# Kernel optimization log

Hardware: AMD Instinct MI355X
Metric: run time of the kernel (lower is better)

## Reference

```python
import jax, jax.numpy as jnp
import numpy as np

N = 40000   # query points
M = 40000   # support points
H = 32      # neighbors per query
CIN = 64
COUT = 64
KS = 3      # kernel points per dim
PDIM = 3
K = KS ** PDIM  # 27 kernel points
RADIUS = 1.0
KP_EXTENT = RADIUS / (KS - 1) * PDIM ** 0.5


def _kernel_points():
    # replicates KPConv.getKernelPoints: grid of KS^PDIM points in a ball of RADIUS
    xyz = np.linspace(-1.0, 1.0, KS)
    pts = np.meshgrid(*PDIM * [xyz])
    pts = np.vstack([p.flatten() for p in pts]).T  # [K, PDIM]
    pts = pts / PDIM ** 0.5
    return (pts * RADIUS).astype(np.float32)


def setup_inputs() -> dict:
    key = jax.random.key(0)
    k1, k2, k3, k4, k5 = jax.random.split(key, 5)
    q_pts = jax.random.uniform(k1, (N, PDIM), dtype=jnp.float32) * 10.0
    s_pts = jax.random.uniform(k2, (M, PDIM), dtype=jnp.float32) * 10.0
    neighb_inds = jax.random.randint(k3, (N, H), 0, M + 1)  # M == shadow index
    x = jax.random.normal(k4, (M, CIN), dtype=jnp.float32)
    # kaiming-uniform-like init for weights [K, CIN, COUT]
    bound = (6.0 / ((1.0 + 5.0) * CIN)) ** 0.5
    weights = jax.random.uniform(k5, (K, CIN, COUT), dtype=jnp.float32,
                                 minval=-bound, maxval=bound)
    kernel_points = jnp.asarray(_kernel_points())
    return {"q_pts": q_pts, "s_pts": s_pts, "neighb_inds": neighb_inds,
            "x": x, "weights": weights, "kernel_points": kernel_points}


def reference(q_pts, s_pts, neighb_inds, x, weights, kernel_points):
    # append shadow support point (far away) and zero shadow feature
    s_pts_p = jnp.concatenate(
        [s_pts, jnp.full((1, s_pts.shape[-1]), 1e6, dtype=s_pts.dtype)], axis=0)
    x_p = jnp.concatenate(
        [x, jnp.zeros((1, x.shape[-1]), dtype=x.dtype)], axis=0)

    neighbors = s_pts_p[neighb_inds] - q_pts[:, None, :]        # [N, H, 3]
    neighb_x = x_p[neighb_inds]                                  # [N, H, CIN]

    # distance of each neighbor to each kernel point
    diff = neighbors[:, :, None, :] - kernel_points              # [N, H, K, 3]
    sq_d = jnp.sum(diff * diff, axis=-1)                         # [N, H, K]
    all_w = jnp.clip(1.0 - jnp.sqrt(sq_d) / KP_EXTENT, 0.0)      # [N, H, K]

    # all_weights^T @ neighb_x  -> [N, K, CIN]
    weighted = jnp.einsum('nhk,nhc->nkc', all_w, neighb_x)
    # per-kernel-point matmul with weights [K, CIN, COUT], summed over K
    out = jnp.einsum('nkc,kco->no', weighted, weights)           # [N, COUT]
    return out
```

## Files before the change

### kernel.cpp

```cpp
#include <hip/hip_runtime.h>

typedef short bf16x8 __attribute__((ext_vector_type(8)));
typedef float f32x4  __attribute__((ext_vector_type(4)));

#define HN    32
#define CIN   64
#define KP    27
#define QB    64
#define CAPB  96
#define NTB   1024
#define OSTR  65

#define QB2   32
#define CAP2  64
#define OSTR2 68

#define INV_EXT 1.1547005383792517f
#define CUT2    3.4821f

__device__ __forceinline__ unsigned f2bf(float f){
    union{float fv;unsigned u;}v; v.fv=f;
    unsigned u=v.u;
    u += 0x7fffu + ((u>>16)&1u);
    return u>>16;
}

__global__ __launch_bounds__(256)
void kp_prep2(const float* __restrict__ s, const float* __restrict__ W,
              float4* __restrict__ o, unsigned short* __restrict__ Wt2, int M)
{
    int tid = blockIdx.x*256 + threadIdx.x;
    if (tid < M) o[tid] = make_float4(s[tid*3+0], s[tid*3+1], s[tid*3+2], 0.f);
    if (tid < KP*8*64){
        int lane = tid & 63;
        int f  = (tid>>6) & 7;
        int kk = tid >> 9;
        int ot = f>>1, ks = f&1, gg = lane>>4;
        unsigned r[8];
#pragma unroll
        for (int j=0;j<8;++j)
            r[j] = f2bf(W[(size_t)kk*4096 + (size_t)(ks*32 + gg*8 + j)*64 + ot*16 + (lane&15)]);
        uint4 v; v.x=r[0]|(r[1]<<16); v.y=r[2]|(r[3]<<16); v.z=r[4]|(r[5]<<16); v.w=r[6]|(r[7]<<16);
        *(uint4*)&Wt2[(size_t)tid*8] = v;
    }
}

__device__ __forceinline__ void loadB(const unsigned short* __restrict__ Wt2, int k, int lane,
                                      bf16x8 (&b)[8]){
    const unsigned short* base = Wt2 + ((size_t)(k*8)*64 + lane)*8;
#pragma unroll
    for (int f=0;f<8;++f) b[f] = *(const bf16x8*)(base + f*512);
}
__device__ __forceinline__ void loadB_w(const float* __restrict__ W, int k, int lane, int g,
                                        bf16x8 (&b)[8]){
#pragma unroll
    for (int f=0;f<8;++f){
        int ot=f>>1, ks=f&1;
        union{unsigned u[4]; bf16x8 v;} bb;
#pragma unroll
        for (int jj=0;jj<4;++jj){
            unsigned l0=f2bf(W[(size_t)k*4096 + (size_t)(ks*32+g*8+2*jj)*64   + ot*16+(lane&15)]);
            unsigned l1=f2bf(W[(size_t)k*4096 + (size_t)(ks*32+g*8+2*jj+1)*64 + ot*16+(lane&15)]);
            bb.u[jj]=l0|(l1<<16);
        }
        b[f]=bb.v;
    }
}

__global__ __launch_bounds__(256,4)
void kpconv_fused(const float* __restrict__ q_pts, const int* __restrict__ inds,
                  const float* __restrict__ x, const float* __restrict__ kpts,
                  const float4* __restrict__ sp4, const unsigned short* __restrict__ Wt2,
                  float* __restrict__ out, int N, int M)
{
    __shared__ unsigned short rows[64*CIN];
    __shared__ __align__(16) float wlds[KP*64];
    __shared__ __align__(16) float outacc[QB2*OSTR2];
    __shared__ float qls[QB2*3];
    __shared__ float bx[CAP2], by[CAP2], bz[CAP2];
    __shared__ int bq[CAP2], bixs[CAP2];
    __shared__ int cnt;

    const int t    = threadIdx.x;
    const int lane = t & 63;
    const int wv   = t >> 6;
    const int g    = lane >> 4;
    const int r15  = lane & 15;
    const int nq0  = blockIdx.x * QB2;
    const int NP   = N*HN;

    for (int j=t; j<QB2*OSTR2; j+=256) outacc[j]=0.f;
    for (int j=t; j<QB2*3;    j+=256){ int gi=nq0*3+j; qls[j]=(gi<N*3)? q_pts[gi]:0.f; }
    if (t < CAP2) bq[t]=0;
    if (t==0) cnt=0;
    __syncthreads();

    int idxv[4];
#pragma unroll
    for (int jj=0; jj<4; ++jj){
        int pair = nq0*HN + jj*256 + t;
        idxv[jj] = (pair < NP) ? inds[pair] : M;
    }
    float4 s4v[4];
#pragma unroll
    for (int jj=0; jj<4; ++jj){
        int ic = (idxv[jj] < M) ? idxv[jj] : 0;
        s4v[jj] = sp4[ic];
    }
#pragma unroll
    for (int jj=0; jj<4; ++jj){
        if (idxv[jj] < M){
            int q = (jj*256 + t) >> 5;
            float px=s4v[jj].x-qls[q*3], py=s4v[jj].y-qls[q*3+1], pz=s4v[jj].z-qls[q*3+2];
            if (px*px+py*py+pz*pz <= CUT2){
                int sl = atomicAdd(&cnt, 1);
                if (sl < CAP2){ bx[sl]=px; by[sl]=py; bz[sl]=pz; bq[sl]=q; bixs[sl]=idxv[jj]; }
            }
        }
    }
    __syncthreads();
    const int total = cnt;

    auto process = [&](int cc){
        const int nrow = (cc + 15) & ~15;
        int itA=t, itB=t+256;
        int rlA=itA>>3, c8A=itA&7, rlB=itB>>3, c8B=itB&7;
        bool vA=(rlA<cc), vB=(rlB<cc);
        bool wrA=(rlA<nrow), wrB=(rlB<nrow);
        int ixA = vA ? bixs[rlA] : bixs[0];
        int ixB = vB ? bixs[rlB] : bixs[0];
        const float4* xrA = (const float4*)(x + (size_t)ixA*CIN);
        const float4* xrB = (const float4*)(x + (size_t)ixB*CIN);
        float4 fA0=xrA[c8A*2], fA1=xrA[c8A*2+1];
        float4 fB0=xrB[c8B*2], fB1=xrB[c8B*2+1];
        for (int i=t; i<KP*64; i+=256){
            int row = i&63;
            if (row >= nrow) continue;
            int k = i>>6;
            float w=0.f;
            if (row < cc){
                float dx=bx[row]-kpts[k*3+0];
                float dy=by[row]-kpts[k*3+1];
                float dz=bz[row]-kpts[k*3+2];
                w = fmaxf(1.f - sqrtf(dx*dx+dy*dy+dz*dz)*INV_EXT, 0.f);
            }
            wlds[i]=w;
        }
        if (wrA){
            uint4 v; v.x=0u; v.y=0u; v.z=0u; v.w=0u;
            if (vA){
                v.x=f2bf(fA0.x)|(f2bf(fA0.y)<<16); v.y=f2bf(fA0.z)|(f2bf(fA0.w)<<16);
                v.z=f2bf(fA1.x)|(f2bf(fA1.y)<<16); v.w=f2bf(fA1.z)|(f2bf(fA1.w)<<16);
            }
            *(uint4*)((char*)rows + rlA*128 + ((c8A*16)^((rlA&7)<<4))) = v;
        }
        if (wrB){
            uint4 v; v.x=0u; v.y=0u; v.z=0u; v.w=0u;
            if (vB){
                v.x=f2bf(fB0.x)|(f2bf(fB0.y)<<16); v.y=f2bf(fB0.z)|(f2bf(fB0.w)<<16);
                v.z=f2bf(fB1.x)|(f2bf(fB1.y)<<16); v.w=f2bf(fB1.z)|(f2bf(fB1.w)<<16);
            }
            *(uint4*)((char*)rows + rlB*128 + ((c8B*16)^((rlB&7)<<4))) = v;
        }
        __syncthreads();

        const char* rb = (const char*)rows;
        for (int ch=0; ch*32 < cc; ++ch){
            bool rtv[2];
            bf16x8 A0[2], A1[2];
#pragma unroll
            for (int rt=0; rt<2; ++rt){
                rtv[rt] = (ch*32 + rt*16) < cc;
                int row = ch*32 + rt*16 + r15;
                int rc  = rtv[rt] ? row : r15;
                A0[rt] = *(const bf16x8*)(rb + rc*128 + (( g*16)   ^((rc&7)<<4)));
                A1[rt] = *(const bf16x8*)(rb + rc*128 + ((64+g*16) ^((rc&7)<<4)));
            }
            f32x4 acc[2][4];
#pragma unroll
            for (int rt=0; rt<2; ++rt)
#pragma unroll
                for (int ot=0; ot<4; ++ot){ f32x4 z={0.f,0.f,0.f,0.f}; acc[rt][ot]=z; }

#pragma unroll 1
            for (int j=0; j<7; ++j){
                int k = wv + 4*j;
                bool hask = (k < KP);
                int kl = hask ? k : 0;
                bf16x8 B[8];
                loadB(Wt2, kl, lane, B);
                const float* wk = &wlds[kl*64 + ch*32];
                f32x4 w4[2];
#pragma unroll
                for (int rt=0; rt<2; ++rt){
                    f32x4 z={0.f,0.f,0.f,0.f};
                    if (rtv[rt]) z = *(const f32x4*)(wk + rt*16 + g*4);
                    w4[rt]=z;
                }
                if (!hask) continue;
#pragma unroll
                for (int rt=0; rt<2; ++rt){
                    bool act = rtv[rt] && __any(w4[rt][0]>0.f || w4[rt][1]>0.f ||
                                                w4[rt][2]>0.f || w4[rt][3]>0.f);
                    if (act){
#pragma unroll
                        for (int ot=0; ot<4; ++ot){
                            f32x4 c={0.f,0.f,0.f,0.f};
                            c = __builtin_amdgcn_mfma_f32_16x16x32_bf16(A0[rt], B[2*ot  ], c, 0,0,0);
                            c = __builtin_amdgcn_mfma_f32_16x16x32_bf16(A1[rt], B[2*ot+1], c, 0,0,0);
                            acc[rt][ot][0] += w4[rt][0]*c[0];
                            acc[rt][ot][1] += w4[rt][1]*c[1];
                            acc[rt][ot][2] += w4[rt][2]*c[2];
                            acc[rt][ot][3] += w4[rt][3]*c[3];
                        }
                    }
                }
            }
#pragma unroll
            for (int rt=0; rt<2; ++rt){
                if (!rtv[rt]) continue;
                int rbase = ch*32 + rt*16 + g*4;
#pragma unroll
                for (int rr=0; rr<4; ++rr){
                    int qv = bq[rbase+rr];
#pragma unroll
                    for (int ot=0; ot<4; ++ot){
                        float val = acc[rt][ot][rr];
                        if (val != 0.f)
                            atomicAdd(&outacc[qv*OSTR2 + ot*16 + r15], val);
                    }
                }
            }
        }
        __syncthreads();
    };

    if (total <= CAP2){
        if (total > 0) process(total);
    } else {
        for (int w=0; w<(QB2*HN)/64; ++w){
            __syncthreads();
            if (t==0) cnt=0;
            __syncthreads();
            if (t < 64){
                int pl = w*64 + t, pair = nq0*HN + pl;
                if (pair < NP){
                    int idx = inds[pair];
                    if ((unsigned)idx < (unsigned)M){
                        int q = pl >> 5;
                        float4 s4 = sp4[idx];
                        float px=s4.x-qls[q*3], py=s4.y-qls[q*3+1], pz=s4.z-qls[q*3+2];
                        if (px*px+py*py+pz*pz <= CUT2){
                            int sl = atomicAdd(&cnt, 1);
                            bx[sl]=px; by[sl]=py; bz[sl]=pz; bq[sl]=q; bixs[sl]=idx;
                        }
                    }
                }
            }
            __syncthreads();
            if (cnt > 0) process(cnt);
        }
    }
    __syncthreads();

    for (int j=t; j<QB2*16; j+=256){
        int q=j>>4, o4=j&15, n=nq0+q;
        if (n < N)
            ((float4*)out)[(size_t)n*16 + o4] = *(const float4*)&outacc[q*OSTR2 + o4*4];
    }
}


__global__ __launch_bounds__(NTB)
void kpconv6(const float* __restrict__ q_pts, const float* __restrict__ s_pts,
             const int* __restrict__ inds, const float* __restrict__ x,
             const float* __restrict__ W, const float* __restrict__ kpts,
             float* __restrict__ out, int N, int M)
{
    __shared__ float qls[QB*3];
    __shared__ float posx[CAPB], posy[CAPB], posz[CAPB];
    __shared__ int   eqb[CAPB], eidxb[CAPB];
    __shared__ unsigned short rows[CAPB*CIN];
    __shared__ float outacc[QB*OSTR];
    __shared__ int   cnt;

    const int t    = threadIdx.x;
    const int lane = t & 63;
    const int wv   = t >> 6;
    const int g    = lane >> 4;
    const int r15  = lane & 15;
    const int nq0  = blockIdx.x * QB;

    const int k0 = wv, k1 = wv + 16;
    const bool has2 = (k1 < KP);

    bf16x8 B0[8], B1[8];
    loadB_w(W, k0, lane, g, B0);
    loadB_w(W, has2 ? k1 : k0, lane, g, B1);
    const float k0x=kpts[k0*3+0], k0y=kpts[k0*3+1], k0z=kpts[k0*3+2];
    float k1x=0.f,k1y=0.f,k1z=0.f;
    if (has2){ k1x=kpts[k1*3+0]; k1y=kpts[k1*3+1]; k1z=kpts[k1*3+2]; }

    for (int j=t; j<QB*OSTR; j+=NTB) outacc[j]=0.f;
    for (int j=t; j<QB*3;   j+=NTB){ int gi=nq0*3+j; qls[j]=(gi<N*3)? q_pts[gi]:0.f; }
    if (t==0) cnt=0;
    __syncthreads();

    auto process = [&](int cc){
        if (cc<=0) return;
        const int ntile=(cc+15)>>4, nrow=ntile*16;
        for (int j=cc+t; j<nrow; j+=NTB){ posx[j]=1e9f; posy[j]=1e9f; posz[j]=1e9f; eqb[j]=0; }
        for (int it=t; it<nrow*8; it+=NTB){
            int e=it>>3, c8=it&7;
            uint4 v; v.x=0u; v.y=0u; v.z=0u; v.w=0u;
            if (e<cc){
                const float4* xr=(const float4*)(x+(size_t)eidxb[e]*CIN);
                float4 f0=xr[c8*2], f1=xr[c8*2+1];
                v.x=f2bf(f0.x)|(f2bf(f0.y)<<16); v.y=f2bf(f0.z)|(f2bf(f0.w)<<16);
                v.z=f2bf(f1.x)|(f2bf(f1.y)<<16); v.w=f2bf(f1.z)|(f2bf(f1.w)<<16);
            }
            int ba=e*128+((c8*16)^((e&7)<<4));
            *(uint4*)((char*)rows+ba)=v;
        }
        __syncthreads();
        for (int tile=0; tile<ntile; ++tile){
            const char* rb=(const char*)rows;
            int row=tile*16+r15;
            bf16x8 a0=*(const bf16x8*)(rb+row*128+((g*16)    ^((row&7)<<4)));
            bf16x8 a1=*(const bf16x8*)(rb+row*128+((64+g*16) ^((row&7)<<4)));
            int rbase=tile*16+g*4;
            float w0[4], w1[4]; int qq[4];
#pragma unroll
            for (int r=0;r<4;++r){
                float sx=posx[rbase+r], sy=posy[rbase+r], sz=posz[rbase+r];
                qq[r]=eqb[rbase+r];
                float dx=sx-k0x, dy=sy-k0y, dz=sz-k0z;
                w0[r]=fmaxf(1.f-sqrtf(dx*dx+dy*dy+dz*dz)*INV_EXT,0.f);
                float ex=sx-k1x, ey=sy-k1y, ez=sz-k1z;
                float w1r=fmaxf(1.f-sqrtf(ex*ex+ey*ey+ez*ez)*INV_EXT,0.f);
                w1[r]=has2? w1r : 0.f;
            }
#pragma unroll
            for (int ot=0;ot<4;++ot){
                f32x4 c={0.f,0.f,0.f,0.f};
                c=__builtin_amdgcn_mfma_f32_16x16x32_bf16(a0,B0[2*ot],c,0,0,0);
                c=__builtin_amdgcn_mfma_f32_16x16x32_bf16(a1,B0[2*ot+1],c,0,0,0);
                f32x4 d={0.f,0.f,0.f,0.f};
                if (has2){
                    d=__builtin_amdgcn_mfma_f32_16x16x32_bf16(a0,B1[2*ot],d,0,0,0);
                    d=__builtin_amdgcn_mfma_f32_16x16x32_bf16(a1,B1[2*ot+1],d,0,0,0);
                }
#pragma unroll
                for (int r=0;r<4;++r){
                    float val=w0[r]*c[r]+w1[r]*d[r];
                    if (val!=0.f) atomicAdd(&outacc[qq[r]*OSTR+ot*16+r15], val);
                }
            }
        }
        __syncthreads();
    };

    for (int it=t; it<QB*HN; it+=NTB){
        int q=it>>5, h=it&31, n=nq0+q;
        bool inr=false; int idx=0; float px=0.f,py=0.f,pz=0.f;
        if (n<N){
            idx=inds[(size_t)n*HN+h];
            if ((unsigned)idx<(unsigned)M){
                float sx=s_pts[idx*3], sy=s_pts[idx*3+1], sz=s_pts[idx*3+2];
                px=sx-qls[q*3]; py=sy-qls[q*3+1]; pz=sz-qls[q*3+2];
                inr=(px*px+py*py+pz*pz)<=CUT2;
            }
        }
        if (inr){
            int sl=atomicAdd(&cnt,1);
            if (sl<CAPB){ eqb[sl]=q; eidxb[sl]=idx; posx[sl]=px; posy[sl]=py; posz[sl]=pz; }
        }
    }
    __syncthreads();
    const int total=cnt;

    if (total<=CAPB){
        process(total);
    } else {
        for (int w=0; w<(QB*HN)/64; ++w){
            __syncthreads();
            if (t==0) cnt=0;
            __syncthreads();
            if (t<64){
                int pair=w*64+t;
                int q=pair>>5, h=pair&31, n=nq0+q;
                if (n<N){
                    int idx=inds[(size_t)n*HN+h];
                    if ((unsigned)idx<(unsigned)M){
                        float sx=s_pts[idx*3], sy=s_pts[idx*3+1], sz=s_pts[idx*3+2];
                        float px=sx-qls[q*3], py=sy-qls[q*3+1], pz=sz-qls[q*3+2];
                        if (px*px+py*py+pz*pz<=CUT2){
                            int sl=atomicAdd(&cnt,1);
                            eqb[sl]=q; eidxb[sl]=idx; posx[sl]=px; posy[sl]=py; posz[sl]=pz;
                        }
                    }
                }
            }
            __syncthreads();
            process(cnt);
        }
    }
    __syncthreads();

    for (int j=t; j<QB*CIN; j+=NTB){
        int q=j>>6, o=j&63, n=nq0+q;
        if (n<N) out[(size_t)n*CIN+o]=outacc[q*OSTR+o];
    }
}

extern "C" void kernel_launch(void* const* d_in, const int* in_sizes, int n_in,
                              void* d_out, int out_size, void* d_ws, size_t ws_size,
                              hipStream_t stream)
{
    const float* q_pts=(const float*)d_in[0];
    const float* s_pts=(const float*)d_in[1];
    const int*   inds =(const int*)d_in[2];
    const float* x    =(const float*)d_in[3];
    const float* W    =(const float*)d_in[4];
    const float* kpts =(const float*)d_in[5];
    float* outp=(float*)d_out;
    int N=in_sizes[0]/3;
    int M=in_sizes[1]/3;

    char* wsb=(char*)d_ws;
    float4* sp4=(float4*)wsb;
    unsigned short* Wt2=(unsigned short*)(wsb + (size_t)M*16);

    const size_t WT2B = (size_t)KP*8*64*8*2;
    size_t need = (size_t)M*16 + WT2B;

    if (ws_size >= need){
        int prepN = (M > KP*8*64) ? M : KP*8*64;
        hipLaunchKernelGGL(kp_prep2, dim3((prepN+255)/256), dim3(256), 0, stream,
                           s_pts, W, sp4, Wt2, M);
        int nblocks = (N + QB2 - 1) / QB2;
        hipLaunchKernelGGL(kpconv_fused, dim3(nblocks), dim3(256), 0, stream,
                           q_pts, inds, x, kpts, sp4, Wt2, outp, N, M);
        return;
    }

    hipLaunchKernelGGL(kpconv6, dim3((N+QB-1)/QB), dim3(NTB), 0, stream,
                       q_pts, s_pts, inds, x, W, kpts, outp, N, M);
}
```

Baseline: 51.43 us.

## Split fused KPConv MFMA work across waves by output tile and kernel half

```diff
diff --git a/kernel.cpp b/kernel.cpp
--- a/kernel.cpp
+++ b/kernel.cpp
@@ -11,8 +11,10 @@
 #define NTB   1024
 #define OSTR  65
 
-#define QB2   32
-#define CAP2  64
+#define QB2   64
+#define NT2   512
+#define CAP2  96
+#define WL    96
 #define OSTR2 68
 
 #define INV_EXT 1.1547005383792517f
@@ -45,11 +47,8 @@
     }
 }
 
-__device__ __forceinline__ void loadB(const unsigned short* __restrict__ Wt2, int k, int lane,
-                                      bf16x8 (&b)[8]){
-    const unsigned short* base = Wt2 + ((size_t)(k*8)*64 + lane)*8;
-#pragma unroll
-    for (int f=0;f<8;++f) b[f] = *(const bf16x8*)(base + f*512);
+__device__ __forceinline__ bf16x8 ldBf(const unsigned short* __restrict__ Wt2, int k, int f, int lane){
+    return *(const bf16x8*)(Wt2 + ((size_t)(k*8 + f)*64 + lane)*8);
 }
 __device__ __forceinline__ void loadB_w(const float* __restrict__ W, int k, int lane, int g,
                                         bf16x8 (&b)[8]){
@@ -67,14 +66,14 @@
     }
 }
 
-__global__ __launch_bounds__(256,4)
+__global__ __launch_bounds__(NT2,4)
 void kpconv_fused(const float* __restrict__ q_pts, const int* __restrict__ inds,
                   const float* __restrict__ x, const float* __restrict__ kpts,
                   const float4* __restrict__ sp4, const unsigned short* __restrict__ Wt2,
                   float* __restrict__ out, int N, int M)
 {
-    __shared__ unsigned short rows[64*CIN];
-    __shared__ __align__(16) float wlds[KP*64];
+    __shared__ unsigned short rows[CAP2*CIN];
+    __shared__ __align__(16) float wlds[KP*WL];
     __shared__ __align__(16) float outacc[QB2*OSTR2];
     __shared__ float qls[QB2*3];
     __shared__ float bx[CAP2], by[CAP2], bz[CAP2];
@@ -84,13 +83,15 @@
     const int t    = threadIdx.x;
     const int lane = t & 63;
     const int wv   = t >> 6;
+    const int ot   = wv & 3;
+    const int kh   = wv >> 2;
     const int g    = lane >> 4;
     const int r15  = lane & 15;
     const int nq0  = blockIdx.x * QB2;
     const int NP   = N*HN;
 
-    for (int j=t; j<QB2*OSTR2; j+=256) outacc[j]=0.f;
-    for (int j=t; j<QB2*3;    j+=256){ int gi=nq0*3+j; qls[j]=(gi<N*3)? q_pts[gi]:0.f; }
+    for (int j=t; j<QB2*OSTR2; j+=NT2) outacc[j]=0.f;
+    for (int j=t; j<QB2*3;    j+=NT2){ int gi=nq0*3+j; qls[j]=(gi<N*3)? q_pts[gi]:0.f; }
     if (t < CAP2) bq[t]=0;
     if (t==0) cnt=0;
     __syncthreads();
@@ -98,7 +99,7 @@
     int idxv[4];
 #pragma unroll
     for (int jj=0; jj<4; ++jj){
-        int pair = nq0*HN + jj*256 + t;
+        int pair = nq0*HN + jj*NT2 + t;
         idxv[jj] = (pair < NP) ? inds[pair] : M;
     }
     float4 s4v[4];
@@ -110,7 +111,7 @@
 #pragma unroll
     for (int jj=0; jj<4; ++jj){
         if (idxv[jj] < M){
-            int q = (jj*256 + t) >> 5;
+            int q = (jj*NT2 + t) >> 5;
             float px=s4v[jj].x-qls[q*3], py=s4v[jj].y-qls[q*3+1], pz=s4v[jj].z-qls[q*3+2];
             if (px*px+py*py+pz*pz <= CUT2){
                 int sl = atomicAdd(&cnt, 1);
@@ -123,7 +124,7 @@
 
     auto process = [&](int cc){
         const int nrow = (cc + 15) & ~15;
-        int itA=t, itB=t+256;
+        int itA=t, itB=t+NT2;
         int rlA=itA>>3, c8A=itA&7, rlB=itB>>3, c8B=itB&7;
         bool vA=(rlA<cc), vB=(rlB<cc);
         bool wrA=(rlA<nrow), wrB=(rlB<nrow);
@@ -133,18 +134,16 @@
         const float4* xrB = (const float4*)(x + (size_t)ixB*CIN);
         float4 fA0=xrA[c8A*2], fA1=xrA[c8A*2+1];
         float4 fB0=xrB[c8B*2], fB1=xrB[c8B*2+1];
-        for (int i=t; i<KP*64; i+=256){
-            int row = i&63;
-            if (row >= nrow) continue;
-            int k = i>>6;
-            float w=0.f;
-            if (row < cc){
-                float dx=bx[row]-kpts[k*3+0];
-                float dy=by[row]-kpts[k*3+1];
-                float dz=bz[row]-kpts[k*3+2];
-                w = fmaxf(1.f - sqrtf(dx*dx+dy*dy+dz*dz)*INV_EXT, 0.f);
-            }
-            wlds[i]=w;
+        for (int k = wv; k < KP; k += 8){
+            float kx=kpts[k*3+0], ky=kpts[k*3+1], kz=kpts[k*3+2];
+            for (int row = lane; row < nrow; row += 64){
+                float w=0.f;
+                if (row < cc){
+                    float dx=bx[row]-kx, dy=by[row]-ky, dz=bz[row]-kz;
+                    w = fmaxf(1.f - sqrtf(dx*dx+dy*dy+dz*dz)*INV_EXT, 0.f);
+                }
+                wlds[k*WL + row]=w;
+            }
         }
         if (wrA){
             uint4 v; v.x=0u; v.y=0u; v.z=0u; v.w=0u;
@@ -165,6 +164,8 @@
         __syncthreads();
 
         const char* rb = (const char*)rows;
+        const int f0 = ot*2, f1 = ot*2+1;
+        const int nk = (KP - kh + 1) >> 1;
         for (int ch=0; ch*32 < cc; ++ch){
             bool rtv[2];
             bf16x8 A0[2], A1[2];
@@ -176,45 +177,35 @@
                 A0[rt] = *(const bf16x8*)(rb + rc*128 + (( g*16)   ^((rc&7)<<4)));
                 A1[rt] = *(const bf16x8*)(rb + rc*128 + ((64+g*16) ^((rc&7)<<4)));
             }
-            f32x4 acc[2][4];
-#pragma unroll
-            for (int rt=0; rt<2; ++rt)
-#pragma unroll
-                for (int ot=0; ot<4; ++ot){ f32x4 z={0.f,0.f,0.f,0.f}; acc[rt][ot]=z; }
-
+            f32x4 acc[2];
+#pragma unroll
+            for (int rt=0; rt<2; ++rt){ f32x4 z={0.f,0.f,0.f,0.f}; acc[rt]=z; }
+
+            bf16x8 Bc0 = ldBf(Wt2, kh, f0, lane);
+            bf16x8 Bc1 = ldBf(Wt2, kh, f1, lane);
 #pragma unroll 1
-            for (int j=0; j<7; ++j){
-                int k = wv + 4*j;
-                bool hask = (k < KP);
-                int kl = hask ? k : 0;
-                bf16x8 B[8];
-                loadB(Wt2, kl, lane, B);
-                const float* wk = &wlds[kl*64 + ch*32];
-                f32x4 w4[2];
+            for (int j=0; j<nk; ++j){
+                int k  = kh + 2*j;
+                int kn = (j+1 < nk) ? (k+2) : k;
+                bf16x8 Bn0 = ldBf(Wt2, kn, f0, lane);
+                bf16x8 Bn1 = ldBf(Wt2, kn, f1, lane);
+                const float* wk = &wlds[k*WL + ch*32];
 #pragma unroll
                 for (int rt=0; rt<2; ++rt){
-                    f32x4 z={0.f,0.f,0.f,0.f};
-                    if (rtv[rt]) z = *(const f32x4*)(wk + rt*16 + g*4);
-                    w4[rt]=z;
-                }
-                if (!hask) continue;
-#pragma unroll
-                for (int rt=0; rt<2; ++rt){
-                    bool act = rtv[rt] && __any(w4[rt][0]>0.f || w4[rt][1]>0.f ||
-                                                w4[rt][2]>0.f || w4[rt][3]>0.f);
+                    if (!rtv[rt]) continue;
+                    f32x4 w4 = *(const f32x4*)(wk + rt*16 + g*4);
+                    bool act = __any(w4[0]>0.f || w4[1]>0.f || w4[2]>0.f || w4[3]>0.f);
                     if (act){
-#pragma unroll
-                        for (int ot=0; ot<4; ++ot){
-                            f32x4 c={0.f,0.f,0.f,0.f};
-                            c = __builtin_amdgcn_mfma_f32_16x16x32_bf16(A0[rt], B[2*ot  ], c, 0,0,0);
-                            c = __builtin_amdgcn_mfma_f32_16x16x32_bf16(A1[rt], B[2*ot+1], c, 0,0,0);
-                            acc[rt][ot][0] += w4[rt][0]*c[0];
-                            acc[rt][ot][1] += w4[rt][1]*c[1];
-                            acc[rt][ot][2] += w4[rt][2]*c[2];
-                            acc[rt][ot][3] += w4[rt][3]*c[3];
-                        }
+                        f32x4 c={0.f,0.f,0.f,0.f};
+                        c = __builtin_amdgcn_mfma_f32_16x16x32_bf16(A0[rt], Bc0, c, 0,0,0);
+                        c = __builtin_amdgcn_mfma_f32_16x16x32_bf16(A1[rt], Bc1, c, 0,0,0);
+                        acc[rt][0] += w4[0]*c[0];
+                        acc[rt][1] += w4[1]*c[1];
+                        acc[rt][2] += w4[2]*c[2];
+                        acc[rt][3] += w4[3]*c[3];
                     }
                 }
+                Bc0 = Bn0; Bc1 = Bn1;
             }
 #pragma unroll
             for (int rt=0; rt<2; ++rt){
@@ -222,13 +213,10 @@
                 int rbase = ch*32 + rt*16 + g*4;
 #pragma unroll
                 for (int rr=0; rr<4; ++rr){
+                    float val = acc[rt][rr];
                     int qv = bq[rbase+rr];
-#pragma unroll
-                    for (int ot=0; ot<4; ++ot){
-                        float val = acc[rt][ot][rr];
-                        if (val != 0.f)
-                            atomicAdd(&outacc[qv*OSTR2 + ot*16 + r15], val);
-                    }
+                    if (val != 0.f)
+                        atomicAdd(&outacc[qv*OSTR2 + ot*16 + r15], val);
                 }
             }
         }
@@ -263,7 +251,7 @@
     }
     __syncthreads();
 
-    for (int j=t; j<QB2*16; j+=256){
+    for (int j=t; j<QB2*16; j+=NT2){
         int q=j>>4, o4=j&15, n=nq0+q;
         if (n < N)
             ((float4*)out)[(size_t)n*16 + o4] = *(const float4*)&outacc[q*OSTR2 + o4*4];
@@ -439,7 +427,7 @@
         hipLaunchKernelGGL(kp_prep2, dim3((prepN+255)/256), dim3(256), 0, stream,
                            s_pts, W, sp4, Wt2, M);
         int nblocks = (N + QB2 - 1) / QB2;
-        hipLaunchKernelGGL(kpconv_fused, dim3(nblocks), dim3(256), 0, stream,
+        hipLaunchKernelGGL(kpconv_fused, dim3(nblocks), dim3(NT2), 0, stream,
                            q_pts, inds, x, kpts, sp4, Wt2, outp, N, M);
         return;
     }
```

After: 55.19 us. +7.3%, slower.

## Split waves over output tiles instead of kernel points, prefetch B fragments

Applied to the files above, without the earlier changes.

```diff
diff --git a/kernel.cpp b/kernel.cpp
--- a/kernel.cpp
+++ b/kernel.cpp
@@ -45,11 +45,8 @@
     }
 }
 
-__device__ __forceinline__ void loadB(const unsigned short* __restrict__ Wt2, int k, int lane,
-                                      bf16x8 (&b)[8]){
-    const unsigned short* base = Wt2 + ((size_t)(k*8)*64 + lane)*8;
-#pragma unroll
-    for (int f=0;f<8;++f) b[f] = *(const bf16x8*)(base + f*512);
+__device__ __forceinline__ bf16x8 ldBf(const unsigned short* __restrict__ Wt2, int k, int f, int lane){
+    return *(const bf16x8*)(Wt2 + ((size_t)(k*8 + f)*64 + lane)*8);
 }
 __device__ __forceinline__ void loadB_w(const float* __restrict__ W, int k, int lane, int g,
                                         bf16x8 (&b)[8]){
@@ -165,71 +162,59 @@
         __syncthreads();
 
         const char* rb = (const char*)rows;
-        for (int ch=0; ch*32 < cc; ++ch){
-            bool rtv[2];
-            bf16x8 A0[2], A1[2];
-#pragma unroll
-            for (int rt=0; rt<2; ++rt){
-                rtv[rt] = (ch*32 + rt*16) < cc;
-                int row = ch*32 + rt*16 + r15;
-                int rc  = rtv[rt] ? row : r15;
-                A0[rt] = *(const bf16x8*)(rb + rc*128 + (( g*16)   ^((rc&7)<<4)));
-                A1[rt] = *(const bf16x8*)(rb + rc*128 + ((64+g*16) ^((rc&7)<<4)));
-            }
-            f32x4 acc[2][4];
-#pragma unroll
-            for (int rt=0; rt<2; ++rt)
-#pragma unroll
-                for (int ot=0; ot<4; ++ot){ f32x4 z={0.f,0.f,0.f,0.f}; acc[rt][ot]=z; }
-
+        bool rtv[4];
+        bf16x8 A0[4], A1[4];
+#pragma unroll
+        for (int rt=0; rt<4; ++rt){
+            rtv[rt] = (rt*16) < cc;
+            int row = rt*16 + r15;
+            int rc  = rtv[rt] ? row : r15;
+            A0[rt] = *(const bf16x8*)(rb + rc*128 + (( g*16)   ^((rc&7)<<4)));
+            A1[rt] = *(const bf16x8*)(rb + rc*128 + ((64+g*16) ^((rc&7)<<4)));
+        }
+        f32x4 acc[4];
+#pragma unroll
+        for (int rt=0; rt<4; ++rt){ f32x4 z={0.f,0.f,0.f,0.f}; acc[rt]=z; }
+
+        const int f0 = wv*2, f1 = wv*2+1;
+        bf16x8 Ba0 = ldBf(Wt2, 0, f0, lane);
+        bf16x8 Ba1 = ldBf(Wt2, 0, f1, lane);
+        bf16x8 Bb0 = ldBf(Wt2, 1, f0, lane);
+        bf16x8 Bb1 = ldBf(Wt2, 1, f1, lane);
 #pragma unroll 1
-            for (int j=0; j<7; ++j){
-                int k = wv + 4*j;
-                bool hask = (k < KP);
-                int kl = hask ? k : 0;
-                bf16x8 B[8];
-                loadB(Wt2, kl, lane, B);
-                const float* wk = &wlds[kl*64 + ch*32];
-                f32x4 w4[2];
-#pragma unroll
-                for (int rt=0; rt<2; ++rt){
-                    f32x4 z={0.f,0.f,0.f,0.f};
-                    if (rtv[rt]) z = *(const f32x4*)(wk + rt*16 + g*4);
-                    w4[rt]=z;
+        for (int k=0; k<KP; ++k){
+            int kf = (k+2 < KP) ? (k+2) : k;
+            bf16x8 Bf0 = ldBf(Wt2, kf, f0, lane);
+            bf16x8 Bf1 = ldBf(Wt2, kf, f1, lane);
+            const float* wk = &wlds[k*64];
+#pragma unroll
+            for (int rt=0; rt<4; ++rt){
+                if (!rtv[rt]) continue;
+                f32x4 w4 = *(const f32x4*)(wk + rt*16 + g*4);
+                bool act = __any(w4[0]>0.f || w4[1]>0.f || w4[2]>0.f || w4[3]>0.f);
+                if (act){
+                    f32x4 c={0.f,0.f,0.f,0.f};
+                    c = __builtin_amdgcn_mfma_f32_16x16x32_bf16(A0[rt], Ba0, c, 0,0,0);
+                    c = __builtin_amdgcn_mfma_f32_16x16x32_bf16(A1[rt], Ba1, c, 0,0,0);
+                    acc[rt][0] += w4[0]*c[0];
+                    acc[rt][1] += w4[1]*c[1];
+                    acc[rt][2] += w4[2]*c[2];
+                    acc[rt][3] += w4[3]*c[3];
                 }
-                if (!hask) continue;
-#pragma unroll
-                for (int rt=0; rt<2; ++rt){
-                    bool act = rtv[rt] && __any(w4[rt][0]>0.f || w4[rt][1]>0.f ||
-                                                w4[rt][2]>0.f || w4[rt][3]>0.f);
-                    if (act){
-#pragma unroll
-                        for (int ot=0; ot<4; ++ot){
-                            f32x4 c={0.f,0.f,0.f,0.f};
-                            c = __builtin_amdgcn_mfma_f32_16x16x32_bf16(A0[rt], B[2*ot  ], c, 0,0,0);
-                            c = __builtin_amdgcn_mfma_f32_16x16x32_bf16(A1[rt], B[2*ot+1], c, 0,0,0);
-                            acc[rt][ot][0] += w4[rt][0]*c[0];
-                            acc[rt][ot][1] += w4[rt][1]*c[1];
-                            acc[rt][ot][2] += w4[rt][2]*c[2];
-                            acc[rt][ot][3] += w4[rt][3]*c[3];
-                        }
-                    }
-                }
-            }
-#pragma unroll
-            for (int rt=0; rt<2; ++rt){
-                if (!rtv[rt]) continue;
-                int rbase = ch*32 + rt*16 + g*4;
-#pragma unroll
-                for (int rr=0; rr<4; ++rr){
-                    int qv = bq[rbase+rr];
-#pragma unroll
-                    for (int ot=0; ot<4; ++ot){
-                        float val = acc[rt][ot][rr];
-                        if (val != 0.f)
-                            atomicAdd(&outacc[qv*OSTR2 + ot*16 + r15], val);
-                    }
-                }
+            }
+            Ba0 = Bb0; Ba1 = Bb1;
+            Bb0 = Bf0; Bb1 = Bf1;
+        }
+#pragma unroll
+        for (int rt=0; rt<4; ++rt){
+            if (!rtv[rt]) continue;
+            int rbase = rt*16 + g*4;
+#pragma unroll
+            for (int rr=0; rr<4; ++rr){
+                float val = acc[rt][rr];
+                int qv = bq[rbase+rr];
+                if (val != 0.f)
+                    atomicAdd(&outacc[qv*OSTR2 + wv*16 + r15], val);
             }
         }
         __syncthreads();
```

New measurement: 46.73 us. 9.1% less time.
